# Performance work log

Hardware: AMD Instinct MI355X
Metric: run time of the kernel (lower is better)

The kernel has to match this reference:

```python
import jax, jax.numpy as jnp
import numpy as np

N = 50000        # nodes
E = 600000       # edges
D_IN = 128       # node_in_channels
H = 256          # hidden_channels
G = 128          # graphs per batch
OUT = 1


def setup_inputs() -> dict:
    key = jax.random.key(0)
    ks = jax.random.split(key, 16)

    def lin(k, fan_in, fan_out):
        k1, k2 = jax.random.split(k)
        bound = 1.0 / np.sqrt(fan_in)
        W = jax.random.uniform(k1, (fan_in, fan_out), jnp.float32, -bound, bound)
        b = jax.random.uniform(k2, (fan_out,), jnp.float32, -bound, bound)
        return W, b

    x = jax.random.normal(ks[0], (N, D_IN), jnp.float32)
    edge_index = jax.random.randint(ks[1], (2, E), 0, N, jnp.int64)
    batch = jnp.sort(jax.random.randint(ks[2], (N,), 0, G, jnp.int64))

    W1, b1 = lin(ks[3], D_IN, H)   # conv1 mlp layer 1
    W2, b2 = lin(ks[4], H, H)      # conv1 mlp layer 2
    W3, b3 = lin(ks[5], H, H)      # conv2 mlp layer 1
    W4, b4 = lin(ks[6], H, H)      # conv2 mlp layer 2
    Wf1, bf1 = lin(ks[7], 2 * H, H)
    Wf2, bf2 = lin(ks[8], H, OUT)

    return {"x": x, "edge_index": edge_index, "batch": batch,
            "W1": W1, "b1": b1, "W2": W2, "b2": b2,
            "W3": W3, "b3": b3, "W4": W4, "b4": b4,
            "Wf1": Wf1, "bf1": bf1, "Wf2": Wf2, "bf2": bf2}


def _gin_conv(h, src, dst, Wa, ba, Wb, bb):
    # GINConv with eps=0: mlp(h + sum_{u->v} h[u])
    agg = jax.ops.segment_sum(h[src], dst, num_segments=h.shape[0])
    z = h + agg
    z = jax.nn.relu(z @ Wa + ba) @ Wb + bb
    return z


def reference(x, edge_index, batch,
              W1, b1, W2, b2, W3, b3, W4, b4,
              Wf1, bf1, Wf2, bf2):
    src, dst = edge_index[0], edge_index[1]

    h = jax.nn.relu(_gin_conv(x, src, dst, W1, b1, W2, b2))
    h = jax.nn.relu(_gin_conv(h, src, dst, W3, b3, W4, b4))

    # global mean / max pooling over graphs
    counts = jax.ops.segment_sum(jnp.ones((h.shape[0],), h.dtype), batch,
                                 num_segments=G)
    sums = jax.ops.segment_sum(h, batch, num_segments=G)
    mean = sums / jnp.maximum(counts, 1.0)[:, None]
    mx = jax.ops.segment_max(h, batch, num_segments=G)
    mx = jnp.where(counts[:, None] > 0, mx, 0.0)

    p = jnp.concatenate([mean, mx], axis=1)          # [G, 2H]
    out = jax.nn.relu(p @ Wf1 + bf1) @ Wf2 + bf2     # [G, OUT]
    return out
```

## Files before the change

kernel.cpp:

```cpp
#include <hip/hip_runtime.h>
#include <math.h>

#define D_IN 128
#define HDIM 256
#define PSPLIT 8

typedef __attribute__((ext_vector_type(8))) short bf16x8;
typedef __attribute__((ext_vector_type(4))) float f32x4;

#define GLOBAL_AS __attribute__((address_space(1)))
#define LDS_AS    __attribute__((address_space(3)))

__device__ __forceinline__ void gload16(const void* g, void* l) {
    __builtin_amdgcn_global_load_lds((const GLOBAL_AS void*)g, (LDS_AS void*)l, 16, 0, 0);
}

__device__ inline ushort f2bf(float v) {
    union { float f; unsigned u; } c; c.f = v;
    unsigned u = c.u;
    return (ushort)((u + 0x7FFFu + ((u >> 16) & 1u)) >> 16);
}
__device__ inline float bf2f(ushort h) {
    union { unsigned u; float f; } c; c.u = ((unsigned)h) << 16; return c.f;
}

__global__ __launch_bounds__(256) void zero_int_kernel(int* __restrict__ p, int n) {
    int i = blockIdx.x * 256 + threadIdx.x;
    int stride = gridDim.x * 256;
    for (; i < n; i += stride) p[i] = 0;
}

__global__ __launch_bounds__(256) void hist_kernel(
    const int* __restrict__ ei, int* __restrict__ deg, int E)
{
    int e = blockIdx.x * 256 + threadIdx.x;
    if (e < E) atomicAdd(&deg[ei[E + e]], 1);
}

__global__ __launch_bounds__(256) void scan_local_kernel(
    const int* __restrict__ deg, int* __restrict__ rowptr,
    int* __restrict__ bsum, int N)
{
    __shared__ int sh[256];
    const int t = threadIdx.x;
    const int i = blockIdx.x * 256 + t;
    int v = (i < N) ? deg[i] : 0;
    sh[t] = v;
    __syncthreads();
#pragma unroll
    for (int off = 1; off < 256; off <<= 1) {
        int x = (t >= off) ? sh[t - off] : 0;
        __syncthreads();
        sh[t] += x;
        __syncthreads();
    }
    if (i < N) rowptr[i] = sh[t] - v;
    if (t == 255) bsum[blockIdx.x] = sh[255];
}

__global__ __launch_bounds__(256) void scan_bsum_kernel(
    int* __restrict__ bsum, int* __restrict__ rowptr, int nb, int N)
{
    __shared__ int sh[256];
    const int t = threadIdx.x;
    int v = (t < nb) ? bsum[t] : 0;
    sh[t] = v;
    __syncthreads();
#pragma unroll
    for (int off = 1; off < 256; off <<= 1) {
        int x = (t >= off) ? sh[t - off] : 0;
        __syncthreads();
        sh[t] += x;
        __syncthreads();
    }
    if (t < nb) bsum[t] = sh[t] - v;
    if (t == 255) rowptr[N] = sh[255];
}

__global__ __launch_bounds__(256) void scan_apply_kernel(
    int* __restrict__ rowptr, int* __restrict__ cursor,
    const int* __restrict__ bsum, int N)
{
    int i = blockIdx.x * 256 + threadIdx.x;
    if (i < N) {
        int v = rowptr[i] + bsum[blockIdx.x];
        rowptr[i] = v;
        cursor[i] = v;
    }
}

__global__ __launch_bounds__(256) void fill_kernel(
    const int* __restrict__ ei, int* __restrict__ cursor,
    int* __restrict__ srclist, int E)
{
    int e = blockIdx.x * 256 + threadIdx.x;
    if (e < E) {
        int s = ei[e];
        int d = ei[E + e];
        int pos = atomicAdd(&cursor[d], 1);
        srclist[pos] = s;
    }
}

template<int K>
__global__ __launch_bounds__(256) void wsplit_kernel(
    const float* __restrict__ W, ushort* __restrict__ Wthi, ushort* __restrict__ Wtlo)
{
    int idx = blockIdx.x * 256 + threadIdx.x;
    if (idx >= K * 256) return;
    int k = idx >> 8;
    int c = idx & 255;
    float v = W[idx];
    ushort h = f2bf(v);
    Wthi[c * K + k] = h;
    Wtlo[c * K + k] = f2bf(v - bf2f(h));
}

__global__ __launch_bounds__(256) void gather1_kernel(
    const float* __restrict__ feat, const int* __restrict__ rowptr,
    const int* __restrict__ srclist, ushort* __restrict__ Zhi,
    ushort* __restrict__ Zlo, int N)
{
    const int wid  = (blockIdx.x * 256 + threadIdx.x) >> 6;
    const int lane = threadIdx.x & 63;
    const int node = wid * 2 + (lane >> 5);
    if (node >= N) return;
    const int lo_ = rowptr[node], hi_ = rowptr[node + 1];
    const int c = (lane & 31) * 4;
    float4 a = *(const float4*)(feat + (size_t)node * D_IN + c);
    float s0 = a.x, s1 = a.y, s2 = a.z, s3 = a.w;
    int i = lo_;
    for (; i + 4 <= hi_; i += 4) {
        int n0 = srclist[i], n1 = srclist[i + 1], n2 = srclist[i + 2], n3 = srclist[i + 3];
        float4 v0 = *(const float4*)(feat + (size_t)n0 * D_IN + c);
        float4 v1 = *(const float4*)(feat + (size_t)n1 * D_IN + c);
        float4 v2 = *(const float4*)(feat + (size_t)n2 * D_IN + c);
        float4 v3 = *(const float4*)(feat + (size_t)n3 * D_IN + c);
        s0 += v0.x + v1.x + v2.x + v3.x;
        s1 += v0.y + v1.y + v2.y + v3.y;
        s2 += v0.z + v1.z + v2.z + v3.z;
        s3 += v0.w + v1.w + v2.w + v3.w;
    }
    for (; i < hi_; ++i) {
        int s = srclist[i];
        float4 v = *(const float4*)(feat + (size_t)s * D_IN + c);
        s0 += v.x; s1 += v.y; s2 += v.z; s3 += v.w;
    }
    ushort h0 = f2bf(s0), h1 = f2bf(s1), h2 = f2bf(s2), h3 = f2bf(s3);
    ushort l0 = f2bf(s0 - bf2f(h0)), l1 = f2bf(s1 - bf2f(h1));
    ushort l2 = f2bf(s2 - bf2f(h2)), l3 = f2bf(s3 - bf2f(h3));
    size_t o = (size_t)node * D_IN + c;
    uint2 oh, ol;
    oh.x = (unsigned)h0 | ((unsigned)h1 << 16); oh.y = (unsigned)h2 | ((unsigned)h3 << 16);
    ol.x = (unsigned)l0 | ((unsigned)l1 << 16); ol.y = (unsigned)l2 | ((unsigned)l3 << 16);
    *(uint2*)(Zhi + o) = oh;
    *(uint2*)(Zlo + o) = ol;
}

__global__ __launch_bounds__(256) void gather2_kernel(
    const float* __restrict__ F, const int* __restrict__ rowptr,
    const int* __restrict__ srclist,
    ushort* __restrict__ Zhi, ushort* __restrict__ Zlo, int N)
{
    const int node = (blockIdx.x * 256 + threadIdx.x) >> 6;
    const int lane = threadIdx.x & 63;
    if (node >= N) return;
    const int lo_ = rowptr[node], hi_ = rowptr[node + 1];
    const int c = lane * 4;
    float4 a = *(const float4*)(F + (size_t)node * HDIM + c);
    float s0 = a.x, s1 = a.y, s2 = a.z, s3 = a.w;
    int i = lo_;
    for (; i + 4 <= hi_; i += 4) {
        int n0 = srclist[i], n1 = srclist[i + 1], n2 = srclist[i + 2], n3 = srclist[i + 3];
        float4 v0 = *(const float4*)(F + (size_t)n0 * HDIM + c);
        float4 v1 = *(const float4*)(F + (size_t)n1 * HDIM + c);
        float4 v2 = *(const float4*)(F + (size_t)n2 * HDIM + c);
        float4 v3 = *(const float4*)(F + (size_t)n3 * HDIM + c);
        s0 += v0.x + v1.x + v2.x + v3.x;
        s1 += v0.y + v1.y + v2.y + v3.y;
        s2 += v0.z + v1.z + v2.z + v3.z;
        s3 += v0.w + v1.w + v2.w + v3.w;
    }
    for (; i < hi_; ++i) {
        int s = srclist[i];
        float4 v = *(const float4*)(F + (size_t)s * HDIM + c);
        s0 += v.x; s1 += v.y; s2 += v.z; s3 += v.w;
    }
    ushort h0 = f2bf(s0), h1 = f2bf(s1), h2 = f2bf(s2), h3 = f2bf(s3);
    ushort l0 = f2bf(s0 - bf2f(h0)), l1 = f2bf(s1 - bf2f(h1));
    ushort l2 = f2bf(s2 - bf2f(h2)), l3 = f2bf(s3 - bf2f(h3));
    size_t o = (size_t)node * HDIM + c;
    uint2 oh, ol;
    oh.x = (unsigned)h0 | ((unsigned)h1 << 16); oh.y = (unsigned)h2 | ((unsigned)h3 << 16);
    ol.x = (unsigned)l0 | ((unsigned)l1 << 16); ol.y = (unsigned)l2 | ((unsigned)l3 << 16);
    *(uint2*)(Zhi + o) = oh;
    *(uint2*)(Zlo + o) = ol;
}

template<int K, bool SPLIT_OUT>
__global__ __launch_bounds__(256) void mfma_gemm_kernel(
    const ushort* __restrict__ Ahi, const ushort* __restrict__ Alo,
    const ushort* __restrict__ Bthi, const ushort* __restrict__ Btlo,
    const float* __restrict__ Bias, float* __restrict__ OUTf,
    ushort* __restrict__ OUThi, ushort* __restrict__ OUTlo, int Nrows)
{
    __shared__ ushort As[2][64][32];
    __shared__ ushort Ws[2][256][32];
    const int t    = threadIdx.x;
    const int wv   = t >> 6;
    const int lane = t & 63;
    const int l15  = lane & 15;
    const int l4   = lane >> 4;
    const int row0 = blockIdx.x * 64;
    const int wc0  = wv * 64;

    const int srow   = lane >> 2;
    const int schunk = (lane & 3) ^ ((lane >> 3) & 3);
    const int rchunk = (l4 ^ ((l15 >> 1) & 3)) * 8;

    f32x4 acc[4][4];
#pragma unroll
    for (int m = 0; m < 4; ++m)
#pragma unroll
        for (int n = 0; n < 4; ++n) acc[m][n] = (f32x4){0.f, 0.f, 0.f, 0.f};

    const int agrow = min(row0 + wv * 16 + srow, Nrows - 1);
    const size_t abase = (size_t)agrow * K + schunk * 8;

    for (int k0 = 0; k0 < K; k0 += 32) {
#pragma unroll
        for (int j = 0; j < 4; ++j) {
            const int g = wv * 4 + j;
            const size_t wb = (size_t)(g * 16 + srow) * K + k0 + schunk * 8;
            gload16(Bthi + wb, &Ws[0][g * 16][0]);
            gload16(Btlo + wb, &Ws[1][g * 16][0]);
        }
        gload16(Ahi + abase + k0, &As[0][wv * 16][0]);
        gload16(Alo + abase + k0, &As[1][wv * 16][0]);
        __syncthreads();

        bf16x8 ah[4], al[4], bh[4], bl[4];
#pragma unroll
        for (int m = 0; m < 4; ++m) {
            ah[m] = *(const bf16x8*)&As[0][m * 16 + l15][rchunk];
            al[m] = *(const bf16x8*)&As[1][m * 16 + l15][rchunk];
        }
#pragma unroll
        for (int n = 0; n < 4; ++n) {
            bh[n] = *(const bf16x8*)&Ws[0][wc0 + n * 16 + l15][rchunk];
            bl[n] = *(const bf16x8*)&Ws[1][wc0 + n * 16 + l15][rchunk];
        }
#pragma unroll
        for (int m = 0; m < 4; ++m)
#pragma unroll
            for (int n = 0; n < 4; ++n) {
                acc[m][n] = __builtin_amdgcn_mfma_f32_16x16x32_bf16(ah[m], bh[n], acc[m][n], 0, 0, 0);
                acc[m][n] = __builtin_amdgcn_mfma_f32_16x16x32_bf16(ah[m], bl[n], acc[m][n], 0, 0, 0);
                acc[m][n] = __builtin_amdgcn_mfma_f32_16x16x32_bf16(al[m], bh[n], acc[m][n], 0, 0, 0);
            }
        __syncthreads();
    }

#pragma unroll
    for (int n = 0; n < 4; ++n) {
        const int ocol = wc0 + n * 16 + l15;
        const float bs = Bias[ocol];
#pragma unroll
        for (int m = 0; m < 4; ++m) {
#pragma unroll
            for (int r = 0; r < 4; ++r) {
                int orow = row0 + m * 16 + l4 * 4 + r;
                if (orow < Nrows) {
                    float v = fmaxf(acc[m][n][r] + bs, 0.f);
                    size_t o = (size_t)orow * HDIM + ocol;
                    if (SPLIT_OUT) {
                        ushort h = f2bf(v);
                        OUThi[o] = h;
                        OUTlo[o] = f2bf(v - bf2f(h));
                    } else {
                        OUTf[o] = v;
                    }
                }
            }
        }
    }
}

__global__ __launch_bounds__(256) void pool_partial_kernel(
    const float* __restrict__ h2, const int* __restrict__ batch,
    float* __restrict__ psum, float* __restrict__ pmax, int N)
{
    const int g = blockIdx.x / PSPLIT;
    const int s = blockIdx.x % PSPLIT;
    const int t = threadIdx.x;

    __shared__ int s_bounds[2];
    if (t < 2) {
        int target = g + t;
        int lo = 0, hi = N;
        while (lo < hi) {
            int mid = (lo + hi) >> 1;
            if (batch[mid] < target) lo = mid + 1; else hi = mid;
        }
        s_bounds[t] = lo;
    }
    __syncthreads();
    const int glo = s_bounds[0], ghi = s_bounds[1];
    const int cnt = ghi - glo;
    const int chunk = (cnt + PSPLIT - 1) / PSPLIT;
    const int clo = glo + s * chunk;
    const int chi = min(clo + chunk, ghi);

    float s0 = 0.f, s1 = 0.f, s2 = 0.f, s3 = 0.f;
    float m0 = -INFINITY, m1 = -INFINITY, m2 = -INFINITY, m3 = -INFINITY;
    int n = clo;
    for (; n + 4 <= chi; n += 4) {
        float v0 = h2[(size_t)(n + 0) * HDIM + t];
        float v1 = h2[(size_t)(n + 1) * HDIM + t];
        float v2 = h2[(size_t)(n + 2) * HDIM + t];
        float v3 = h2[(size_t)(n + 3) * HDIM + t];
        s0 += v0; m0 = fmaxf(m0, v0);
        s1 += v1; m1 = fmaxf(m1, v1);
        s2 += v2; m2 = fmaxf(m2, v2);
        s3 += v3; m3 = fmaxf(m3, v3);
    }
    for (; n < chi; ++n) {
        float v = h2[(size_t)n * HDIM + t];
        s0 += v; m0 = fmaxf(m0, v);
    }
    size_t o = (size_t)blockIdx.x * HDIM + t;
    psum[o] = (s0 + s1) + (s2 + s3);
    pmax[o] = fmaxf(fmaxf(m0, m1), fmaxf(m2, m3));
}

__global__ __launch_bounds__(256) void pool_final_kernel(
    const float* __restrict__ psum, const float* __restrict__ pmax,
    const int* __restrict__ batch,
    const float* __restrict__ Wf1, const float* __restrict__ bf1,
    const float* __restrict__ Wf2, const float* __restrict__ bf2,
    float* __restrict__ out, int N)
{
    const int g = blockIdx.x;
    const int t = threadIdx.x;

    __shared__ int s_bounds[2];
    if (t < 2) {
        int target = g + t;
        int lo = 0, hi = N;
        while (lo < hi) {
            int mid = (lo + hi) >> 1;
            if (batch[mid] < target) lo = mid + 1; else hi = mid;
        }
        s_bounds[t] = lo;
    }
    __syncthreads();
    const int cnt = s_bounds[1] - s_bounds[0];

    float sum = 0.f, mx = -INFINITY;
    const size_t gbase = (size_t)g * PSPLIT * HDIM + t;
#pragma unroll
    for (int s = 0; s < PSPLIT; ++s) {
        sum += psum[gbase + (size_t)s * HDIM];
        mx = fmaxf(mx, pmax[gbase + (size_t)s * HDIM]);
    }

    __shared__ float p[2 * HDIM];
    p[t]        = sum / (float)(cnt > 1 ? cnt : 1);
    p[HDIM + t] = (cnt > 0) ? mx : 0.f;
    __syncthreads();

    float acc = bf1[t];
#pragma unroll 8
    for (int k = 0; k < 2 * HDIM; ++k)
        acc += p[k] * Wf1[k * HDIM + t];
    float hval = fmaxf(acc, 0.f);

    float partial = hval * Wf2[t];
#pragma unroll
    for (int off = 32; off > 0; off >>= 1)
        partial += __shfl_down(partial, off);
    __shared__ float red[4];
    if ((t & 63) == 0) red[t >> 6] = partial;
    __syncthreads();
    if (t == 0) out[g] = red[0] + red[1] + red[2] + red[3] + bf2[0];
}

extern "C" void kernel_launch(void* const* d_in, const int* in_sizes, int n_in,
                              void* d_out, int out_size, void* d_ws, size_t ws_size,
                              hipStream_t stream)
{
    const float* x     = (const float*)d_in[0];
    const int*   ei    = (const int*)d_in[1];
    const int*   batch = (const int*)d_in[2];
    const float* W1 = (const float*)d_in[3];
    const float* b1 = (const float*)d_in[4];
    const float* W2 = (const float*)d_in[5];
    const float* b2 = (const float*)d_in[6];
    const float* W3 = (const float*)d_in[7];
    const float* b3 = (const float*)d_in[8];
    const float* W4 = (const float*)d_in[9];
    const float* b4 = (const float*)d_in[10];
    const float* Wf1 = (const float*)d_in[11];
    const float* bf1 = (const float*)d_in[12];
    const float* Wf2 = (const float*)d_in[13];
    const float* bf2 = (const float*)d_in[14];
    float* out = (float*)d_out;

    const int N  = in_sizes[0] / D_IN;
    const int E  = in_sizes[1] / 2;
    const int Gn = out_size;

    const size_t R = (size_t)N * HDIM;
    float* R0f = (float*)d_ws;
    float* R1f = R0f + R;
    ushort* R0u = (ushort*)R0f;
    ushort* R1u = (ushort*)R1f;

    ushort* wbuf = (ushort*)(R1f + R);
    ushort* W1thi = wbuf;
    ushort* W1tlo = W1thi + 128 * 256;
    ushort* W2thi = W1tlo + 128 * 256;
    ushort* W2tlo = W2thi + 256 * 256;
    ushort* W3thi = W2tlo + 256 * 256;
    ushort* W3tlo = W3thi + 256 * 256;
    ushort* W4thi = W3tlo + 256 * 256;
    ushort* W4tlo = W4thi + 256 * 256;

    int* rowptr  = (int*)(W4tlo + 256 * 256);
    int* cursor  = rowptr + (N + 1);
    int* srclist = cursor + N;
    float* psum  = (float*)(srclist + E);
    float* pmax  = psum + (size_t)Gn * PSPLIT * HDIM;
    int* bsum    = (int*)(pmax + (size_t)Gn * PSPLIT * HDIM);

    const int gblocks  = (N + 63) / 64;
    const int eblocks  = (E + 255) / 256;
    const int wblocks2 = (N + 3) / 4;
    const int wblocks1 = ((N + 1) / 2 + 3) / 4;
    const int nb       = (N + 255) / 256;

    zero_int_kernel<<<64, 256, 0, stream>>>(cursor, N);
    hist_kernel<<<eblocks, 256, 0, stream>>>(ei, cursor, E);
    scan_local_kernel<<<nb, 256, 0, stream>>>(cursor, rowptr, bsum, N);
    scan_bsum_kernel<<<1, 256, 0, stream>>>(bsum, rowptr, nb, N);
    scan_apply_kernel<<<nb, 256, 0, stream>>>(rowptr, cursor, bsum, N);
    fill_kernel<<<eblocks, 256, 0, stream>>>(ei, cursor, srclist, E);

    wsplit_kernel<128><<<128, 256, 0, stream>>>(W1, W1thi, W1tlo);
    wsplit_kernel<256><<<256, 256, 0, stream>>>(W2, W2thi, W2tlo);
    wsplit_kernel<256><<<256, 256, 0, stream>>>(W3, W3thi, W3tlo);
    wsplit_kernel<256><<<256, 256, 0, stream>>>(W4, W4thi, W4tlo);

    ushort* Z1hi = R0u;                 ushort* Z1lo = R0u + (size_t)N * D_IN;
    ushort* T1hi = R1u;                 ushort* T1lo = R1u + R;
    float*  H1   = R0f;
    ushort* Z2hi = R1u;                 ushort* Z2lo = R1u + R;
    ushort* T2hi = R0u;                 ushort* T2lo = R0u + R;
    float*  H2   = R1f;

    gather1_kernel<<<wblocks1, 256, 0, stream>>>(x, rowptr, srclist, Z1hi, Z1lo, N);
    mfma_gemm_kernel<128, true><<<gblocks, 256, 0, stream>>>(
        Z1hi, Z1lo, W1thi, W1tlo, b1, nullptr, T1hi, T1lo, N);
    mfma_gemm_kernel<256, false><<<gblocks, 256, 0, stream>>>(
        T1hi, T1lo, W2thi, W2tlo, b2, H1, nullptr, nullptr, N);

    gather2_kernel<<<wblocks2, 256, 0, stream>>>(H1, rowptr, srclist, Z2hi, Z2lo, N);
    mfma_gemm_kernel<256, true><<<gblocks, 256, 0, stream>>>(
        Z2hi, Z2lo, W3thi, W3tlo, b3, nullptr, T2hi, T2lo, N);
    mfma_gemm_kernel<256, false><<<gblocks, 256, 0, stream>>>(
        T2hi, T2lo, W4thi, W4tlo, b4, H2, nullptr, nullptr, N);

    pool_partial_kernel<<<Gn * PSPLIT, 256, 0, stream>>>(H2, batch, psum, pmax, N);
    pool_final_kernel<<<Gn, 256, 0, stream>>>(psum, pmax, batch,
                                              Wf1, bf1, Wf2, bf2, out, N);
}
```

Measured before the change: 523.3 us.

## Retile GEMM to 128x128 with double-buffered LDS and deepen gather unroll

The split-bf16 MFMA GEMM moves from 64-row x 256-col tiles to 128x128 tiles on a 2D grid, with the four waves in a 2x2 arrangement. LDS staging is double-buffered so the next K-slice's global-to-LDS loads are issued before the current slice's MFMAs, and one barrier per K step is dropped. Both gather kernels unroll neighbor accumulation to 8 loads in flight, with a pairwise add tree. The aim is more reuse per tile, overlap of load latency with compute, and more memory-level parallelism in the gathers, at the cost of more LDS and registers per block.

```diff
diff --git a/kernel.cpp b/kernel.cpp
--- a/kernel.cpp
+++ b/kernel.cpp
@@ -130,16 +130,32 @@
     float4 a = *(const float4*)(feat + (size_t)node * D_IN + c);
     float s0 = a.x, s1 = a.y, s2 = a.z, s3 = a.w;
     int i = lo_;
-    for (; i + 4 <= hi_; i += 4) {
-        int n0 = srclist[i], n1 = srclist[i + 1], n2 = srclist[i + 2], n3 = srclist[i + 3];
+    for (; i + 8 <= hi_; i += 8) {
+        int n0 = srclist[i+0], n1 = srclist[i+1], n2 = srclist[i+2], n3 = srclist[i+3];
+        int n4 = srclist[i+4], n5 = srclist[i+5], n6 = srclist[i+6], n7 = srclist[i+7];
         float4 v0 = *(const float4*)(feat + (size_t)n0 * D_IN + c);
         float4 v1 = *(const float4*)(feat + (size_t)n1 * D_IN + c);
         float4 v2 = *(const float4*)(feat + (size_t)n2 * D_IN + c);
         float4 v3 = *(const float4*)(feat + (size_t)n3 * D_IN + c);
-        s0 += v0.x + v1.x + v2.x + v3.x;
-        s1 += v0.y + v1.y + v2.y + v3.y;
-        s2 += v0.z + v1.z + v2.z + v3.z;
-        s3 += v0.w + v1.w + v2.w + v3.w;
+        float4 v4 = *(const float4*)(feat + (size_t)n4 * D_IN + c);
+        float4 v5 = *(const float4*)(feat + (size_t)n5 * D_IN + c);
+        float4 v6 = *(const float4*)(feat + (size_t)n6 * D_IN + c);
+        float4 v7 = *(const float4*)(feat + (size_t)n7 * D_IN + c);
+        s0 += (v0.x + v1.x) + (v2.x + v3.x) + (v4.x + v5.x) + (v6.x + v7.x);
+        s1 += (v0.y + v1.y) + (v2.y + v3.y) + (v4.y + v5.y) + (v6.y + v7.y);
+        s2 += (v0.z + v1.z) + (v2.z + v3.z) + (v4.z + v5.z) + (v6.z + v7.z);
+        s3 += (v0.w + v1.w) + (v2.w + v3.w) + (v4.w + v5.w) + (v6.w + v7.w);
+    }
+    for (; i + 4 <= hi_; i += 4) {
+        int n0 = srclist[i], n1 = srclist[i+1], n2 = srclist[i+2], n3 = srclist[i+3];
+        float4 v0 = *(const float4*)(feat + (size_t)n0 * D_IN + c);
+        float4 v1 = *(const float4*)(feat + (size_t)n1 * D_IN + c);
+        float4 v2 = *(const float4*)(feat + (size_t)n2 * D_IN + c);
+        float4 v3 = *(const float4*)(feat + (size_t)n3 * D_IN + c);
+        s0 += (v0.x + v1.x) + (v2.x + v3.x);
+        s1 += (v0.y + v1.y) + (v2.y + v3.y);
+        s2 += (v0.z + v1.z) + (v2.z + v3.z);
+        s3 += (v0.w + v1.w) + (v2.w + v3.w);
     }
     for (; i < hi_; ++i) {
         int s = srclist[i];
@@ -170,16 +186,32 @@
     float4 a = *(const float4*)(F + (size_t)node * HDIM + c);
     float s0 = a.x, s1 = a.y, s2 = a.z, s3 = a.w;
     int i = lo_;
-    for (; i + 4 <= hi_; i += 4) {
-        int n0 = srclist[i], n1 = srclist[i + 1], n2 = srclist[i + 2], n3 = srclist[i + 3];
+    for (; i + 8 <= hi_; i += 8) {
+        int n0 = srclist[i+0], n1 = srclist[i+1], n2 = srclist[i+2], n3 = srclist[i+3];
+        int n4 = srclist[i+4], n5 = srclist[i+5], n6 = srclist[i+6], n7 = srclist[i+7];
         float4 v0 = *(const float4*)(F + (size_t)n0 * HDIM + c);
         float4 v1 = *(const float4*)(F + (size_t)n1 * HDIM + c);
         float4 v2 = *(const float4*)(F + (size_t)n2 * HDIM + c);
         float4 v3 = *(const float4*)(F + (size_t)n3 * HDIM + c);
-        s0 += v0.x + v1.x + v2.x + v3.x;
-        s1 += v0.y + v1.y + v2.y + v3.y;
-        s2 += v0.z + v1.z + v2.z + v3.z;
-        s3 += v0.w + v1.w + v2.w + v3.w;
+        float4 v4 = *(const float4*)(F + (size_t)n4 * HDIM + c);
+        float4 v5 = *(const float4*)(F + (size_t)n5 * HDIM + c);
+        float4 v6 = *(const float4*)(F + (size_t)n6 * HDIM + c);
+        float4 v7 = *(const float4*)(F + (size_t)n7 * HDIM + c);
+        s0 += (v0.x + v1.x) + (v2.x + v3.x) + (v4.x + v5.x) + (v6.x + v7.x);
+        s1 += (v0.y + v1.y) + (v2.y + v3.y) + (v4.y + v5.y) + (v6.y + v7.y);
+        s2 += (v0.z + v1.z) + (v2.z + v3.z) + (v4.z + v5.z) + (v6.z + v7.z);
+        s3 += (v0.w + v1.w) + (v2.w + v3.w) + (v4.w + v5.w) + (v6.w + v7.w);
+    }
+    for (; i + 4 <= hi_; i += 4) {
+        int n0 = srclist[i], n1 = srclist[i+1], n2 = srclist[i+2], n3 = srclist[i+3];
+        float4 v0 = *(const float4*)(F + (size_t)n0 * HDIM + c);
+        float4 v1 = *(const float4*)(F + (size_t)n1 * HDIM + c);
+        float4 v2 = *(const float4*)(F + (size_t)n2 * HDIM + c);
+        float4 v3 = *(const float4*)(F + (size_t)n3 * HDIM + c);
+        s0 += (v0.x + v1.x) + (v2.x + v3.x);
+        s1 += (v0.y + v1.y) + (v2.y + v3.y);
+        s2 += (v0.z + v1.z) + (v2.z + v3.z);
+        s3 += (v0.w + v1.w) + (v2.w + v3.w);
     }
     for (; i < hi_; ++i) {
         int s = srclist[i];
@@ -204,15 +236,17 @@
     const float* __restrict__ Bias, float* __restrict__ OUTf,
     ushort* __restrict__ OUThi, ushort* __restrict__ OUTlo, int Nrows)
 {
-    __shared__ ushort As[2][64][32];
-    __shared__ ushort Ws[2][256][32];
+    __shared__ ushort As[2][2][128][32];
+    __shared__ ushort Ws[2][2][128][32];
     const int t    = threadIdx.x;
     const int wv   = t >> 6;
     const int lane = t & 63;
     const int l15  = lane & 15;
     const int l4   = lane >> 4;
-    const int row0 = blockIdx.x * 64;
-    const int wc0  = wv * 64;
+    const int r0   = blockIdx.x * 128;
+    const int c0   = blockIdx.y * 128;
+    const int wr   = (wv >> 1) * 64;
+    const int wc   = (wv & 1) * 64;
 
     const int srow   = lane >> 2;
     const int schunk = (lane & 3) ^ ((lane >> 3) & 3);
@@ -224,31 +258,43 @@
 #pragma unroll
         for (int n = 0; n < 4; ++n) acc[m][n] = (f32x4){0.f, 0.f, 0.f, 0.f};
 
-    const int agrow = min(row0 + wv * 16 + srow, Nrows - 1);
-    const size_t abase = (size_t)agrow * K + schunk * 8;
-
-    for (int k0 = 0; k0 < K; k0 += 32) {
-#pragma unroll
-        for (int j = 0; j < 4; ++j) {
-            const int g = wv * 4 + j;
-            const size_t wb = (size_t)(g * 16 + srow) * K + k0 + schunk * 8;
-            gload16(Bthi + wb, &Ws[0][g * 16][0]);
-            gload16(Btlo + wb, &Ws[1][g * 16][0]);
+    const int g0 = wv * 2, g1 = wv * 2 + 1;
+    const int arow0 = min(r0 + g0 * 16 + srow, Nrows - 1);
+    const int arow1 = min(r0 + g1 * 16 + srow, Nrows - 1);
+    const size_t ab0 = (size_t)arow0 * K + schunk * 8;
+    const size_t ab1 = (size_t)arow1 * K + schunk * 8;
+    const size_t wb0 = (size_t)(c0 + g0 * 16 + srow) * K + schunk * 8;
+    const size_t wb1 = (size_t)(c0 + g1 * 16 + srow) * K + schunk * 8;
+
+#define STAGE(buf, k0)                                          \
+    do {                                                        \
+        gload16(Ahi + ab0 + (k0), &As[buf][0][g0 * 16][0]);     \
+        gload16(Alo + ab0 + (k0), &As[buf][1][g0 * 16][0]);     \
+        gload16(Ahi + ab1 + (k0), &As[buf][0][g1 * 16][0]);     \
+        gload16(Alo + ab1 + (k0), &As[buf][1][g1 * 16][0]);     \
+        gload16(Bthi + wb0 + (k0), &Ws[buf][0][g0 * 16][0]);    \
+        gload16(Btlo + wb0 + (k0), &Ws[buf][1][g0 * 16][0]);    \
+        gload16(Bthi + wb1 + (k0), &Ws[buf][0][g1 * 16][0]);    \
+        gload16(Btlo + wb1 + (k0), &Ws[buf][1][g1 * 16][0]);    \
+    } while (0)
+
+    const int nk = K / 32;
+    STAGE(0, 0);
+    __syncthreads();
+    int cur = 0;
+    for (int s = 0; s < nk; ++s) {
+        if (s + 1 < nk) STAGE(cur ^ 1, (s + 1) * 32);
+
+        bf16x8 ah[4], al[4], bh[4], bl[4];
+#pragma unroll
+        for (int m = 0; m < 4; ++m) {
+            ah[m] = *(const bf16x8*)&As[cur][0][wr + m * 16 + l15][rchunk];
+            al[m] = *(const bf16x8*)&As[cur][1][wr + m * 16 + l15][rchunk];
         }
-        gload16(Ahi + abase + k0, &As[0][wv * 16][0]);
-        gload16(Alo + abase + k0, &As[1][wv * 16][0]);
-        __syncthreads();
-
-        bf16x8 ah[4], al[4], bh[4], bl[4];
-#pragma unroll
-        for (int m = 0; m < 4; ++m) {
-            ah[m] = *(const bf16x8*)&As[0][m * 16 + l15][rchunk];
-            al[m] = *(const bf16x8*)&As[1][m * 16 + l15][rchunk];
-        }
 #pragma unroll
         for (int n = 0; n < 4; ++n) {
-            bh[n] = *(const bf16x8*)&Ws[0][wc0 + n * 16 + l15][rchunk];
-            bl[n] = *(const bf16x8*)&Ws[1][wc0 + n * 16 + l15][rchunk];
+            bh[n] = *(const bf16x8*)&Ws[cur][0][wc + n * 16 + l15][rchunk];
+            bl[n] = *(const bf16x8*)&Ws[cur][1][wc + n * 16 + l15][rchunk];
         }
 #pragma unroll
         for (int m = 0; m < 4; ++m)
@@ -259,17 +305,19 @@
                 acc[m][n] = __builtin_amdgcn_mfma_f32_16x16x32_bf16(al[m], bh[n], acc[m][n], 0, 0, 0);
             }
         __syncthreads();
-    }
+        cur ^= 1;
+    }
+#undef STAGE
 
 #pragma unroll
     for (int n = 0; n < 4; ++n) {
-        const int ocol = wc0 + n * 16 + l15;
+        const int ocol = c0 + wc + n * 16 + l15;
         const float bs = Bias[ocol];
 #pragma unroll
         for (int m = 0; m < 4; ++m) {
 #pragma unroll
             for (int r = 0; r < 4; ++r) {
-                int orow = row0 + m * 16 + l4 * 4 + r;
+                int orow = r0 + wr + m * 16 + l4 * 4 + r;
                 if (orow < Nrows) {
                     float v = fmaxf(acc[m][n][r] + bs, 0.f);
                     size_t o = (size_t)orow * HDIM + ocol;
@@ -433,11 +481,11 @@
     float* pmax  = psum + (size_t)Gn * PSPLIT * HDIM;
     int* bsum    = (int*)(pmax + (size_t)Gn * PSPLIT * HDIM);
 
-    const int gblocks  = (N + 63) / 64;
     const int eblocks  = (E + 255) / 256;
     const int wblocks2 = (N + 3) / 4;
     const int wblocks1 = ((N + 1) / 2 + 3) / 4;
     const int nb       = (N + 255) / 256;
+    const dim3 ggrid((N + 127) / 128, 2);
 
     zero_int_kernel<<<64, 256, 0, stream>>>(cursor, N);
     hist_kernel<<<eblocks, 256, 0, stream>>>(ei, cursor, E);
@@ -459,15 +507,15 @@
     float*  H2   = R1f;
 
     gather1_kernel<<<wblocks1, 256, 0, stream>>>(x, rowptr, srclist, Z1hi, Z1lo, N);
-    mfma_gemm_kernel<128, true><<<gblocks, 256, 0, stream>>>(
+    mfma_gemm_kernel<128, true><<<ggrid, 256, 0, stream>>>(
         Z1hi, Z1lo, W1thi, W1tlo, b1, nullptr, T1hi, T1lo, N);
-    mfma_gemm_kernel<256, false><<<gblocks, 256, 0, stream>>>(
+    mfma_gemm_kernel<256, false><<<ggrid, 256, 0, stream>>>(
         T1hi, T1lo, W2thi, W2tlo, b2, H1, nullptr, nullptr, N);
 
     gather2_kernel<<<wblocks2, 256, 0, stream>>>(H1, rowptr, srclist, Z2hi, Z2lo, N);
-    mfma_gemm_kernel<256, true><<<gblocks, 256, 0, stream>>>(
+    mfma_gemm_kernel<256, true><<<ggrid, 256, 0, stream>>>(
         Z2hi, Z2lo, W3thi, W3tlo, b3, nullptr, T2hi, T2lo, N);
-    mfma_gemm_kernel<256, false><<<gblocks, 256, 0, stream>>>(
+    mfma_gemm_kernel<256, false><<<ggrid, 256, 0, stream>>>(
         T2hi, T2lo, W4thi, W4tlo, b4, H2, nullptr, nullptr, N);
 
     pool_partial_kernel<<<Gn * PSPLIT, 256, 0, stream>>>(H2, batch, psum, pmax, N);
```

Result: slower. 545.7 us (+4.3%).

## Fuse global mean/max pooling into final GEMM epilogue via atomics

Applied to the files above, without the earlier changes.

The last MLP GEMM no longer writes the N×256 fp32 H2 activation. Its epilogue accumulates per-graph segment sums and maxes in registers and flushes them with atomicAdd and unsigned atomicMax into a zeroed G×256 buffer, which removes the separate pool_partial kernel and the H2 round-trip through memory. Because ReLU outputs are non-negative, comparing float bit patterns as unsigned integers gives the correct max, and zero-initialisation stands in for empty graphs. The cost is an extra zeroing launch and contended atomics, while the gather kernels get a small reassociation of their sums.

```diff
diff --git a/kernel.cpp b/kernel.cpp
--- a/kernel.cpp
+++ b/kernel.cpp
@@ -3,7 +3,6 @@
 
 #define D_IN 128
 #define HDIM 256
-#define PSPLIT 8
 
 typedef __attribute__((ext_vector_type(8))) short bf16x8;
 typedef __attribute__((ext_vector_type(4))) float f32x4;
@@ -136,10 +135,10 @@
         float4 v1 = *(const float4*)(feat + (size_t)n1 * D_IN + c);
         float4 v2 = *(const float4*)(feat + (size_t)n2 * D_IN + c);
         float4 v3 = *(const float4*)(feat + (size_t)n3 * D_IN + c);
-        s0 += v0.x + v1.x + v2.x + v3.x;
-        s1 += v0.y + v1.y + v2.y + v3.y;
-        s2 += v0.z + v1.z + v2.z + v3.z;
-        s3 += v0.w + v1.w + v2.w + v3.w;
+        s0 += (v0.x + v1.x) + (v2.x + v3.x);
+        s1 += (v0.y + v1.y) + (v2.y + v3.y);
+        s2 += (v0.z + v1.z) + (v2.z + v3.z);
+        s3 += (v0.w + v1.w) + (v2.w + v3.w);
     }
     for (; i < hi_; ++i) {
         int s = srclist[i];
@@ -176,10 +175,10 @@
         float4 v1 = *(const float4*)(F + (size_t)n1 * HDIM + c);
         float4 v2 = *(const float4*)(F + (size_t)n2 * HDIM + c);
         float4 v3 = *(const float4*)(F + (size_t)n3 * HDIM + c);
-        s0 += v0.x + v1.x + v2.x + v3.x;
-        s1 += v0.y + v1.y + v2.y + v3.y;
-        s2 += v0.z + v1.z + v2.z + v3.z;
-        s3 += v0.w + v1.w + v2.w + v3.w;
+        s0 += (v0.x + v1.x) + (v2.x + v3.x);
+        s1 += (v0.y + v1.y) + (v2.y + v3.y);
+        s2 += (v0.z + v1.z) + (v2.z + v3.z);
+        s3 += (v0.w + v1.w) + (v2.w + v3.w);
     }
     for (; i < hi_; ++i) {
         int s = srclist[i];
@@ -197,12 +196,14 @@
     *(uint2*)(Zlo + o) = ol;
 }
 
-template<int K, bool SPLIT_OUT>
+template<int K, int OMODE>
 __global__ __launch_bounds__(256) void mfma_gemm_kernel(
     const ushort* __restrict__ Ahi, const ushort* __restrict__ Alo,
     const ushort* __restrict__ Bthi, const ushort* __restrict__ Btlo,
     const float* __restrict__ Bias, float* __restrict__ OUTf,
-    ushort* __restrict__ OUThi, ushort* __restrict__ OUTlo, int Nrows)
+    ushort* __restrict__ OUThi, ushort* __restrict__ OUTlo,
+    const int* __restrict__ batch, float* __restrict__ psum,
+    unsigned* __restrict__ pmax, int Nrows)
 {
     __shared__ ushort As[2][64][32];
     __shared__ ushort Ws[2][256][32];
@@ -265,20 +266,47 @@
     for (int n = 0; n < 4; ++n) {
         const int ocol = wc0 + n * 16 + l15;
         const float bs = Bias[ocol];
-#pragma unroll
-        for (int m = 0; m < 4; ++m) {
-#pragma unroll
-            for (int r = 0; r < 4; ++r) {
-                int orow = row0 + m * 16 + l4 * 4 + r;
-                if (orow < Nrows) {
-                    float v = fmaxf(acc[m][n][r] + bs, 0.f);
-                    size_t o = (size_t)orow * HDIM + ocol;
-                    if (SPLIT_OUT) {
-                        ushort h = f2bf(v);
-                        OUThi[o] = h;
-                        OUTlo[o] = f2bf(v - bf2f(h));
-                    } else {
-                        OUTf[o] = v;
+        if (OMODE == 2) {
+            int gcur = -1; float ssum = 0.f; float smax = 0.f;
+#pragma unroll
+            for (int m = 0; m < 4; ++m) {
+#pragma unroll
+                for (int r = 0; r < 4; ++r) {
+                    int orow = row0 + m * 16 + l4 * 4 + r;
+                    if (orow < Nrows) {
+                        float v = fmaxf(acc[m][n][r] + bs, 0.f);
+                        int g = batch[orow];
+                        if (g != gcur) {
+                            if (gcur >= 0) {
+                                atomicAdd(&psum[gcur * HDIM + ocol], ssum);
+                                atomicMax(&pmax[gcur * HDIM + ocol], __float_as_uint(smax));
+                            }
+                            gcur = g; ssum = 0.f; smax = 0.f;
+                        }
+                        ssum += v; smax = fmaxf(smax, v);
+                    }
+                }
+            }
+            if (gcur >= 0) {
+                atomicAdd(&psum[gcur * HDIM + ocol], ssum);
+                atomicMax(&pmax[gcur * HDIM + ocol], __float_as_uint(smax));
+            }
+        } else {
+#pragma unroll
+            for (int m = 0; m < 4; ++m) {
+#pragma unroll
+                for (int r = 0; r < 4; ++r) {
+                    int orow = row0 + m * 16 + l4 * 4 + r;
+                    if (orow < Nrows) {
+                        float v = fmaxf(acc[m][n][r] + bs, 0.f);
+                        size_t o = (size_t)orow * HDIM + ocol;
+                        if (OMODE == 1) {
+                            ushort h = f2bf(v);
+                            OUThi[o] = h;
+                            OUTlo[o] = f2bf(v - bf2f(h));
+                        } else {
+                            OUTf[o] = v;
+                        }
                     }
                 }
             }
@@ -286,12 +314,14 @@
     }
 }
 
-__global__ __launch_bounds__(256) void pool_partial_kernel(
-    const float* __restrict__ h2, const int* __restrict__ batch,
-    float* __restrict__ psum, float* __restrict__ pmax, int N)
-{
-    const int g = blockIdx.x / PSPLIT;
-    const int s = blockIdx.x % PSPLIT;
+__global__ __launch_bounds__(256) void pool_final_kernel(
+    const float* __restrict__ psum, const unsigned* __restrict__ pmax,
+    const int* __restrict__ batch,
+    const float* __restrict__ Wf1, const float* __restrict__ bf1,
+    const float* __restrict__ Wf2, const float* __restrict__ bf2,
+    float* __restrict__ out, int N)
+{
+    const int g = blockIdx.x;
     const int t = threadIdx.x;
 
     __shared__ int s_bounds[2];
@@ -305,68 +335,14 @@
         s_bounds[t] = lo;
     }
     __syncthreads();
-    const int glo = s_bounds[0], ghi = s_bounds[1];
-    const int cnt = ghi - glo;
-    const int chunk = (cnt + PSPLIT - 1) / PSPLIT;
-    const int clo = glo + s * chunk;
-    const int chi = min(clo + chunk, ghi);
-
-    float s0 = 0.f, s1 = 0.f, s2 = 0.f, s3 = 0.f;
-    float m0 = -INFINITY, m1 = -INFINITY, m2 = -INFINITY, m3 = -INFINITY;
-    int n = clo;
-    for (; n + 4 <= chi; n += 4) {
-        float v0 = h2[(size_t)(n + 0) * HDIM + t];
-        float v1 = h2[(size_t)(n + 1) * HDIM + t];
-        float v2 = h2[(size_t)(n + 2) * HDIM + t];
-        float v3 = h2[(size_t)(n + 3) * HDIM + t];
-        s0 += v0; m0 = fmaxf(m0, v0);
-        s1 += v1; m1 = fmaxf(m1, v1);
-        s2 += v2; m2 = fmaxf(m2, v2);
-        s3 += v3; m3 = fmaxf(m3, v3);
-    }
-    for (; n < chi; ++n) {
-        float v = h2[(size_t)n * HDIM + t];
-        s0 += v; m0 = fmaxf(m0, v);
-    }
-    size_t o = (size_t)blockIdx.x * HDIM + t;
-    psum[o] = (s0 + s1) + (s2 + s3);
-    pmax[o] = fmaxf(fmaxf(m0, m1), fmaxf(m2, m3));
-}
-
-__global__ __launch_bounds__(256) void pool_final_kernel(
-    const float* __restrict__ psum, const float* __restrict__ pmax,
-    const int* __restrict__ batch,
-    const float* __restrict__ Wf1, const float* __restrict__ bf1,
-    const float* __restrict__ Wf2, const float* __restrict__ bf2,
-    float* __restrict__ out, int N)
-{
-    const int g = blockIdx.x;
-    const int t = threadIdx.x;
-
-    __shared__ int s_bounds[2];
-    if (t < 2) {
-        int target = g + t;
-        int lo = 0, hi = N;
-        while (lo < hi) {
-            int mid = (lo + hi) >> 1;
-            if (batch[mid] < target) lo = mid + 1; else hi = mid;
-        }
-        s_bounds[t] = lo;
-    }
-    __syncthreads();
     const int cnt = s_bounds[1] - s_bounds[0];
 
-    float sum = 0.f, mx = -INFINITY;
-    const size_t gbase = (size_t)g * PSPLIT * HDIM + t;
-#pragma unroll
-    for (int s = 0; s < PSPLIT; ++s) {
-        sum += psum[gbase + (size_t)s * HDIM];
-        mx = fmaxf(mx, pmax[gbase + (size_t)s * HDIM]);
-    }
+    float sum = psum[g * HDIM + t];
+    float mx  = __uint_as_float(pmax[g * HDIM + t]);
 
     __shared__ float p[2 * HDIM];
     p[t]        = sum / (float)(cnt > 1 ? cnt : 1);
-    p[HDIM + t] = (cnt > 0) ? mx : 0.f;
+    p[HDIM + t] = mx;
     __syncthreads();
 
     float acc = bf1[t];
@@ -429,9 +405,9 @@
     int* rowptr  = (int*)(W4tlo + 256 * 256);
     int* cursor  = rowptr + (N + 1);
     int* srclist = cursor + N;
-    float* psum  = (float*)(srclist + E);
-    float* pmax  = psum + (size_t)Gn * PSPLIT * HDIM;
-    int* bsum    = (int*)(pmax + (size_t)Gn * PSPLIT * HDIM);
+    float* psum     = (float*)(srclist + E);
+    unsigned* pmax  = (unsigned*)(psum + (size_t)Gn * HDIM);
+    int* bsum       = (int*)(pmax + (size_t)Gn * HDIM);
 
     const int gblocks  = (N + 63) / 64;
     const int eblocks  = (E + 255) / 256;
@@ -450,27 +426,26 @@
     wsplit_kernel<256><<<256, 256, 0, stream>>>(W2, W2thi, W2tlo);
     wsplit_kernel<256><<<256, 256, 0, stream>>>(W3, W3thi, W3tlo);
     wsplit_kernel<256><<<256, 256, 0, stream>>>(W4, W4thi, W4tlo);
+    zero_int_kernel<<<64, 256, 0, stream>>>((int*)psum, 2 * Gn * HDIM);
 
     ushort* Z1hi = R0u;                 ushort* Z1lo = R0u + (size_t)N * D_IN;
     ushort* T1hi = R1u;                 ushort* T1lo = R1u + R;
     float*  H1   = R0f;
     ushort* Z2hi = R1u;                 ushort* Z2lo = R1u + R;
     ushort* T2hi = R0u;                 ushort* T2lo = R0u + R;
-    float*  H2   = R1f;
 
     gather1_kernel<<<wblocks1, 256, 0, stream>>>(x, rowptr, srclist, Z1hi, Z1lo, N);
-    mfma_gemm_kernel<128, true><<<gblocks, 256, 0, stream>>>(
-        Z1hi, Z1lo, W1thi, W1tlo, b1, nullptr, T1hi, T1lo, N);
-    mfma_gemm_kernel<256, false><<<gblocks, 256, 0, stream>>>(
-        T1hi, T1lo, W2thi, W2tlo, b2, H1, nullptr, nullptr, N);
+    mfma_gemm_kernel<128, 1><<<gblocks, 256, 0, stream>>>(
+        Z1hi, Z1lo, W1thi, W1tlo, b1, nullptr, T1hi, T1lo, nullptr, nullptr, nullptr, N);
+    mfma_gemm_kernel<256, 0><<<gblocks, 256, 0, stream>>>(
+        T1hi, T1lo, W2thi, W2tlo, b2, H1, nullptr, nullptr, nullptr, nullptr, nullptr, N);
 
     gather2_kernel<<<wblocks2, 256, 0, stream>>>(H1, rowptr, srclist, Z2hi, Z2lo, N);
-    mfma_gemm_kernel<256, true><<<gblocks, 256, 0, stream>>>(
-        Z2hi, Z2lo, W3thi, W3tlo, b3, nullptr, T2hi, T2lo, N);
-    mfma_gemm_kernel<256, false><<<gblocks, 256, 0, stream>>>(
-        T2hi, T2lo, W4thi, W4tlo, b4, H2, nullptr, nullptr, N);
-
-    pool_partial_kernel<<<Gn * PSPLIT, 256, 0, stream>>>(H2, batch, psum, pmax, N);
+    mfma_gemm_kernel<256, 1><<<gblocks, 256, 0, stream>>>(
+        Z2hi, Z2lo, W3thi, W3tlo, b3, nullptr, T2hi, T2lo, nullptr, nullptr, nullptr, N);
+    mfma_gemm_kernel<256, 2><<<gblocks, 256, 0, stream>>>(
+        T2hi, T2lo, W4thi, W4tlo, b4, nullptr, nullptr, nullptr, batch, psum, pmax, N);
+
     pool_final_kernel<<<Gn, 256, 0, stream>>>(psum, pmax, batch,
                                               Wf1, bf1, Wf2, bf2, out, N);
 }
```

Result: no change. 526.5 us (+0.6%).
